# Optimization experiments

Measured on AMD Instinct MI355X. Metric: run time of the kernel, lower is better.

## Reference

```python
import jax, jax.numpy as jnp
import numpy as np
import math

# BDH config (defaults from BDHConfig)
D = 256        # n_embd
NH = 4         # n_head
MULT = 128     # mlp_internal_dim_multiplier
N = MULT * D // NH   # 8192 latent dim per head
NLAYER = 6
VOCAB = 256
B, T = 1, 1024
THETA = 2.0 ** 16
TWO_PI = 2.0 * math.pi


def _freqs(n):
    # get_freqs: quantize exponent to even integers
    t = jnp.arange(n, dtype=jnp.float32)
    q = jnp.floor(t / 2.0) * 2.0
    return 1.0 / (THETA ** (q / n)) / TWO_PI  # [N]


def _ln(x, eps=1e-5):
    # LayerNorm without affine params (elementwise_affine=False)
    m = jnp.mean(x, axis=-1, keepdims=True)
    v = jnp.mean((x - m) ** 2, axis=-1, keepdims=True)
    return (x - m) / jnp.sqrt(v + eps)


def _rope(phases, v):
    # phases: [T,N] broadcastable to v [...,T,N]
    ph = (phases % 1.0) * TWO_PI
    cos, sin = jnp.cos(ph), jnp.sin(ph)
    # rotate adjacent pairs: (-v_odd, v_even) interleaved
    vrot = jnp.stack((-v[..., 1::2], v[..., ::2]), axis=-1).reshape(v.shape)
    return v * cos + vrot * sin


def setup_inputs() -> dict:
    key = jax.random.key(0)
    ks = jax.random.split(key, 6)
    std = 0.02
    return {
        "idx": jax.random.randint(ks[0], (B, T), 0, VOCAB),
        "embed_w": jax.random.normal(ks[1], (VOCAB, D), jnp.float32) * std,
        "encoder": jax.random.normal(ks[2], (NH, D, N), jnp.float32) * std,
        "encoder_v": jax.random.normal(ks[3], (NH, D, N), jnp.float32) * std,
        "decoder": jax.random.normal(ks[4], (NH * N, D), jnp.float32) * std,
        "lm_head": jax.random.normal(ks[5], (D, VOCAB), jnp.float32) * std,
    }


def reference(idx, embed_w, encoder, encoder_v, decoder, lm_head):
    freqs = _freqs(N)                                             # [N]
    phases = jnp.arange(T, dtype=jnp.float32)[:, None] * freqs    # [T,N]
    mask = jnp.tril(jnp.ones((T, T), jnp.float32), k=-1)          # strict causal
    dec = decoder.reshape(NH, N, D)

    x = _ln(embed_w[idx])                                         # [B,T,D]
    for _ in range(NLAYER):
        x_sp = jax.nn.relu(jnp.einsum('btd,hdn->bhtn', x, encoder))   # [B,nh,T,N]
        qr = _rope(phases, x_sp)                                       # [B,nh,T,N]
        scores = jnp.einsum('bhtn,bhsn->bhts', qr, qr) * mask          # [B,nh,T,T]
        ykv = _ln(jnp.einsum('bhts,bsd->bhtd', scores, x))             # [B,nh,T,D]
        y_sp = jax.nn.relu(jnp.einsum('bhtd,hdn->bhtn', ykv, encoder_v))
        xy = x_sp * y_sp                                               # [B,nh,T,N]
        ymlp = jnp.einsum('bhtn,hnd->btd', xy, dec)                    # [B,T,D]
        x = _ln(x + _ln(ymlp))
    return x @ lm_head                                                 # [B,T,VOCAB]
```

## Files before the change

kernel.cpp:

```cpp
#include <hip/hip_runtime.h>
#include <hip/hip_bf16.h>
#include <math.h>

#define T_ 1024
#define D_ 256
#define N_ 8192
#define NH_ 4
#define NLAYER_ 6
#define VOCAB_ 256
#define TWO_PI_F 6.283185307179586f

typedef __attribute__((ext_vector_type(8))) short short8;
typedef __attribute__((ext_vector_type(4))) float floatx4;
typedef unsigned short ushort_t;

__device__ __forceinline__ void cp16(const void* g, void* l) {
    __builtin_amdgcn_global_load_lds((const __attribute__((address_space(1))) unsigned int*)g,
                                     (__attribute__((address_space(3))) unsigned int*)l,
                                     16, 0, 0);
}

__device__ __forceinline__ float bf2f_raw(unsigned short u) {
    union { unsigned int i; float f; } x;
    x.i = ((unsigned int)u) << 16;
    return x.f;
}
__device__ __forceinline__ unsigned int f2bf_u(float f) {
    union { float f; unsigned int u; } x; x.f = f;
    return (x.u + 0x7fffu + ((x.u >> 16) & 1u)) >> 16;
}
__device__ __forceinline__ unsigned int rope_fwd_w(unsigned int vw, unsigned int csw) {
    float ve = bf2f_raw((unsigned short)(vw & 0xffff));
    float vo = bf2f_raw((unsigned short)(vw >> 16));
    float c = bf2f_raw((unsigned short)(csw & 0xffff));
    float s = bf2f_raw((unsigned short)(csw >> 16));
    return f2bf_u(ve * c - vo * s) | (f2bf_u(vo * c + ve * s) << 16);
}
__device__ __forceinline__ unsigned int xy_mul_w(unsigned int vw, unsigned int qw,
                                                 unsigned int csw) {
    float ve = bf2f_raw((unsigned short)(vw & 0xffff));
    float vo = bf2f_raw((unsigned short)(vw >> 16));
    float qe = bf2f_raw((unsigned short)(qw & 0xffff));
    float qo = bf2f_raw((unsigned short)(qw >> 16));
    float c = bf2f_raw((unsigned short)(csw & 0xffff));
    float s = bf2f_raw((unsigned short)(csw >> 16));
    float xe = qe * c + qo * s;
    float xo = qo * c - qe * s;
    return f2bf_u(ve * xe) | (f2bf_u(vo * xo) << 16);
}

__device__ __forceinline__ float block_sum(float v, float* red) {
    int tid = threadIdx.x;
    red[tid] = v;
    __syncthreads();
    #pragma unroll
    for (int s = 128; s > 0; s >>= 1) {
        if (tid < s) red[tid] += red[tid + s];
        __syncthreads();
    }
    float r = red[0];
    __syncthreads();
    return r;
}


__global__ void k_embed_ln(const int* __restrict__ idx, const float* __restrict__ ew,
                           float* __restrict__ x, __hip_bfloat16* __restrict__ x_bf) {
    __shared__ float red[256];
    int t = blockIdx.x, d = threadIdx.x;
    float v = ew[idx[t] * D_ + d];
    float mean = block_sum(v, red) * (1.0f / D_);
    float c = v - mean;
    float var = block_sum(c * c, red) * (1.0f / D_);
    float o = c * rsqrtf(var + 1e-5f);
    x[t * D_ + d] = o;
    x_bf[t * D_ + d] = __float2bfloat16(o);
}

__global__ void k_ln_rows(const float* __restrict__ yp, __hip_bfloat16* __restrict__ outb) {
    __shared__ float red[256];
    int r = blockIdx.x, d = threadIdx.x;
    const size_t S = (size_t)NH_ * T_ * D_;
    float v = yp[(size_t)r * D_ + d] + yp[S + (size_t)r * D_ + d];
    float mean = block_sum(v, red) * (1.0f / D_);
    float c = v - mean;
    float var = block_sum(c * c, red) * (1.0f / D_);
    outb[(size_t)r * D_ + d] = __float2bfloat16(c * rsqrtf(var + 1e-5f));
}

__global__ void k_x_update(float* __restrict__ x, const unsigned int* __restrict__ ypart,
                           __hip_bfloat16* __restrict__ x_bf) {
    __shared__ float red[256];
    int t = blockIdx.x, d = threadIdx.x;
    float v = 0.0f;
    #pragma unroll
    for (int i = 0; i < 32; i++) {
        unsigned int w = ypart[(size_t)i * (T_ * D_ / 2) + t * (D_ / 2) + (d >> 1)];
        v += bf2f_raw((unsigned short)((d & 1) ? (w >> 16) : (w & 0xffff)));
    }
    float m1 = block_sum(v, red) * (1.0f / D_);
    float c1 = v - m1;
    float v1 = block_sum(c1 * c1, red) * (1.0f / D_);
    float u = c1 * rsqrtf(v1 + 1e-5f);
    float w = x[t * D_ + d] + u;
    float m2 = block_sum(w, red) * (1.0f / D_);
    float c2 = w - m2;
    float v2 = block_sum(c2 * c2, red) * (1.0f / D_);
    float o = c2 * rsqrtf(v2 + 1e-5f);
    x[t * D_ + d] = o;
    x_bf[t * D_ + d] = __float2bfloat16(o);
}

__global__ __launch_bounds__(256) void k_tcvt(const float* __restrict__ in,
                                              __hip_bfloat16* __restrict__ out,
                                              int R, int C) {
    int h = blockIdx.z;
    int r0 = blockIdx.y * 32, c0 = blockIdx.x * 32;
    __shared__ float tile[32][33];
    int tx = threadIdx.x & 31, ty = threadIdx.x >> 5;
    const float* inh = in + (size_t)h * R * C;
    __hip_bfloat16* outh = out + (size_t)h * R * C;
    #pragma unroll
    for (int i = 0; i < 4; i++)
        tile[ty + 8 * i][tx] = inh[(size_t)(r0 + ty + 8 * i) * C + c0 + tx];
    __syncthreads();
    #pragma unroll
    for (int i = 0; i < 4; i++)
        outh[(size_t)(c0 + ty + 8 * i) * R + r0 + tx] = __float2bfloat16(tile[tx][ty + 8 * i]);
}

__global__ void k_rope_tab(unsigned int* __restrict__ tab) {
    int idx = blockIdx.x * 256 + threadIdx.x;
    int t = idx >> 12, j = idx & 4095;
    float freq = exp2f((float)j * (-1.0f / 256.0f)) * 0.15915494309189535f;
    float ph = (float)t * freq;
    ph -= floorf(ph);
    float s, c;
    __sincosf(ph * TWO_PI_F, &s, &c);
    tab[idx] = f2bf_u(c) | (f2bf_u(s) << 16);
}

__device__ __forceinline__ void gemm128(const ushort_t* __restrict__ A,
                                        const ushort_t* __restrict__ B,
                                        int lda, int ldb, int K,
                                        ushort_t* As, ushort_t* Bs,
                                        floatx4 acc[4][4]) {
    const int tid = threadIdx.x;
    const int lane = tid & 63, wid = tid >> 6;
    const int wm = wid >> 1, wn = wid & 1;
    const int quad = lane >> 4, col = lane & 15;
    int srow[4], scol[4];
    #pragma unroll
    for (int i = 0; i < 4; i++) {
        int s = i * 256 + tid;
        srow[i] = s >> 3;
        scol[i] = (s & 7) ^ (srow[i] & 7);
    }
    for (int k0 = 0; k0 < K; k0 += 64) {
        #pragma unroll
        for (int i = 0; i < 4; i++)
            cp16(A + (size_t)srow[i] * lda + k0 + scol[i] * 8,
                 As + (size_t)(i * 256 + wid * 64) * 8);
        #pragma unroll
        for (int i = 0; i < 4; i++)
            cp16(B + (size_t)srow[i] * ldb + k0 + scol[i] * 8,
                 Bs + (size_t)(i * 256 + wid * 64) * 8);
        __syncthreads();
        #pragma unroll
        for (int kk = 0; kk < 2; kk++) {
            short8 af[4], bf[4];
            #pragma unroll
            for (int mi = 0; mi < 4; mi++) {
                int row = wm * 64 + mi * 16 + col;
                int pc = ((kk << 2) + quad) ^ (row & 7);
                af[mi] = *(const short8*)&As[row * 64 + pc * 8];
            }
            #pragma unroll
            for (int ni = 0; ni < 4; ni++) {
                int row = wn * 64 + ni * 16 + col;
                int pc = ((kk << 2) + quad) ^ (row & 7);
                bf[ni] = *(const short8*)&Bs[row * 64 + pc * 8];
            }
            #pragma unroll
            for (int mi = 0; mi < 4; mi++)
                #pragma unroll
                for (int ni = 0; ni < 4; ni++)
                    acc[mi][ni] = __builtin_amdgcn_mfma_f32_16x16x32_bf16(
                        af[mi], bf[ni], acc[mi][ni], 0, 0, 0);
        }
        __syncthreads();
    }
}

#define GEMM_PROLOGUE()                                              \
    __shared__ __align__(16) char smem[128 * 65 * 4];                \
    ushort_t* As = (ushort_t*)smem;                                  \
    ushort_t* Bs = (ushort_t*)(smem + 16384);                        \
    unsigned int* sst = (unsigned int*)smem;                         \
    floatx4 acc[4][4];                                               \
    _Pragma("unroll") for (int mi = 0; mi < 4; mi++)                 \
        _Pragma("unroll") for (int ni = 0; ni < 4; ni++)             \
            acc[mi][ni] = (floatx4){0.f, 0.f, 0.f, 0.f};             \
    const int lane = threadIdx.x & 63, wid = threadIdx.x >> 6;       \
    const int wm = wid >> 1, wn = wid & 1;                           \
    const int quad = lane >> 4, col = lane & 15;                     \
    const int odd = lane & 1;                                        \
    const int rsel = odd ? 2 : 0, rother = odd ? 0 : 2;

#define STAGE_PACKED(VALEXPR)                                                 \
    _Pragma("unroll") for (int mi = 0; mi < 4; mi++)                          \
        _Pragma("unroll") for (int ni = 0; ni < 4; ni++) {                    \
            const int w = wn * 32 + ni * 8 + (col >> 1);                      \
            const int lrb = wm * 64 + mi * 16 + quad * 4;                     \
            _Pragma("unroll") for (int rr = 0; rr < 2; rr++) {                \
                int lr_o = lrb + rother + rr;                                 \
                float send = (VALEXPR(acc[mi][ni][rother + rr], lr_o));       \
                float recv = __shfl_xor(send, 1);                             \
                int lr = lrb + rsel + rr;                                     \
                float mine = (VALEXPR(acc[mi][ni][rsel + rr], lr));           \
                float lo = odd ? recv : mine, hi = odd ? mine : recv;         \
                sst[lr * 65 + w] = f2bf_u(lo) | (f2bf_u(hi) << 16);           \
            }                                                                 \
        }                                                                     \
    __syncthreads();

__global__ __launch_bounds__(256) void k_scores_m(const __hip_bfloat16* __restrict__ qr,
                                                  __hip_bfloat16* __restrict__ scp) {
    const int b = blockIdx.x;
    const int ks = b & 3, h = (b >> 2) & 3;
    int i = b >> 4;
    int ti = 0;
    while ((ti + 1) * (ti + 2) / 2 <= i) ti++;
    int si = i - ti * (ti + 1) / 2;
    const int t0 = ti * 128, s0 = si * 128;
    GEMM_PROLOGUE();
    const ushort_t* qh = (const ushort_t*)qr + (size_t)h * T_ * N_ + (size_t)ks * (N_ / 4);
    gemm128(qh + (size_t)t0 * N_, qh + (size_t)s0 * N_, N_, N_, N_ / 4, As, Bs, acc);
    #pragma unroll
    for (int mi = 0; mi < 4; mi++)
        #pragma unroll
        for (int ni = 0; ni < 4; ni++) {
            const int ss = s0 + wn * 64 + ni * 16 + col;
            const int w = wn * 32 + ni * 8 + (col >> 1);
            const int lrb = wm * 64 + mi * 16 + quad * 4;
            #pragma unroll
            for (int rr = 0; rr < 2; rr++) {
                int lr_o = lrb + rother + rr;
                float send = (ss < t0 + lr_o) ? acc[mi][ni][rother + rr] : 0.0f;
                float recv = __shfl_xor(send, 1);
                int lr = lrb + rsel + rr;
                float mine = (ss < t0 + lr) ? acc[mi][ni][rsel + rr] : 0.0f;
                float lo = odd ? recv : mine, hi = odd ? mine : recv;
                sst[lr * 65 + w] = f2bf_u(lo) | (f2bf_u(hi) << 16);
            }
        }
    __syncthreads();
    unsigned int* gb = (unsigned int*)(scp + (size_t)ks * NH_ * T_ * T_ + (size_t)h * T_ * T_)
                       + (size_t)t0 * (T_ / 2) + (s0 >> 1);
    const int tid = threadIdx.x;
    #pragma unroll
    for (int p = 0; p < 8; p++) {
        int g = p * 1024 + tid * 4;
        int lr = g >> 6, w = g & 63;
        uint4 v = make_uint4(sst[lr * 65 + w], sst[lr * 65 + w + 1],
                             sst[lr * 65 + w + 2], sst[lr * 65 + w + 3]);
        *(uint4*)(gb + (size_t)lr * (T_ / 2) + w) = v;
    }
}

__global__ void k_sc_cvt(__hip_bfloat16* __restrict__ scp) {
    int i = blockIdx.x;
    int ti = 0;
    while ((ti + 1) * (ti + 2) / 2 <= i) ti++;
    int si = i - ti * (ti + 1) / 2;
    const size_t S2h = (size_t)NH_ * T_ * T_ / 2;
    unsigned int* sp = (unsigned int*)scp;
    size_t b = (size_t)blockIdx.y * T_ * T_ / 2;
    for (int e = threadIdx.x; e < 128 * 64; e += 256) {
        int r = e >> 6, c = e & 63;
        size_t off = b + (((size_t)(ti * 128 + r) * T_ + si * 128) >> 1) + c;
        float lo = 0.f, hi = 0.f;
        #pragma unroll
        for (int s = 0; s < 4; s++) {
            unsigned int w = sp[off + s * S2h];
            lo += bf2f_raw((unsigned short)(w & 0xffff));
            hi += bf2f_raw((unsigned short)(w >> 16));
        }
        sp[off] = f2bf_u(lo) | (f2bf_u(hi) << 16);
    }
}

#define IDENT_RELU(a, lr) fmaxf((a), 0.0f)
template <int MODE>
__global__ __launch_bounds__(256) void k_proj_m(const __hip_bfloat16* __restrict__ Abf,
                                                const __hip_bfloat16* __restrict__ Wt,
                                                __hip_bfloat16* __restrict__ out1,
                                                const unsigned int* __restrict__ rtab) {
    const int h = blockIdx.z;
    const int t0 = blockIdx.y * 128, n0 = blockIdx.x * 128;
    GEMM_PROLOGUE();
    const ushort_t* Ah = (const ushort_t*)Abf + (MODE ? (size_t)h * T_ * D_ : (size_t)0)
                         + (size_t)t0 * D_;
    const ushort_t* Bh = (const ushort_t*)Wt + (size_t)h * N_ * D_ + (size_t)n0 * D_;
    gemm128(Ah, Bh, D_, D_, D_, As, Bs, acc);
    STAGE_PACKED(IDENT_RELU);
    unsigned int* gb = (unsigned int*)out1 + ((size_t)h * T_ + t0) * (N_ / 2) + (n0 >> 1);
    const unsigned int* rb = rtab + (size_t)t0 * 4096 + (n0 >> 1);
    const int tid = threadIdx.x;
    #pragma unroll
    for (int p = 0; p < 8; p++) {
        int g = p * 1024 + tid * 4;
        int lr = g >> 6, w = g & 63;
        uint4 v = make_uint4(sst[lr * 65 + w], sst[lr * 65 + w + 1],
                             sst[lr * 65 + w + 2], sst[lr * 65 + w + 3]);
        uint4 cs = *(const uint4*)(rb + (size_t)lr * 4096 + w);
        uint4 o;
        if (MODE == 0) {
            o.x = rope_fwd_w(v.x, cs.x); o.y = rope_fwd_w(v.y, cs.y);
            o.z = rope_fwd_w(v.z, cs.z); o.w = rope_fwd_w(v.w, cs.w);
        } else {
            uint4 qw = *(const uint4*)(gb + (size_t)lr * (N_ / 2) + w);
            o.x = xy_mul_w(v.x, qw.x, cs.x); o.y = xy_mul_w(v.y, qw.y, cs.y);
            o.z = xy_mul_w(v.z, qw.z, cs.z); o.w = xy_mul_w(v.w, qw.w, cs.w);
        }
        *(uint4*)(gb + (size_t)lr * (N_ / 2) + w) = o;
    }
}

__global__ __launch_bounds__(256) void k_ykv_m(const __hip_bfloat16* __restrict__ sc,
                                               const __hip_bfloat16* __restrict__ xT,
                                               float* __restrict__ ykvp) {
    const int b = blockIdx.x;
    const int h = (b >> 1) & 3, ks = b & 1;
    const int r0 = b >> 3;
    const int d0 = (r0 & 1) * 128, t0 = (r0 >> 1) * 128;
    GEMM_PROLOGUE();
    const int half = (t0 + 128) >> 1;
    const ushort_t* Ah = (const ushort_t*)sc + (size_t)h * T_ * T_ + (size_t)t0 * T_ + ks * half;
    const ushort_t* Bh = (const ushort_t*)xT + (size_t)d0 * T_ + ks * half;
    gemm128(Ah, Bh, T_, T_, half, As, Bs, acc);
    float2* yp = (float2*)(ykvp + (size_t)ks * NH_ * T_ * D_);
    #pragma unroll
    for (int mi = 0; mi < 4; mi++)
        #pragma unroll
        for (int ni = 0; ni < 4; ni++) {
            const int dd_e = (d0 + wn * 64 + ni * 16 + col) & ~1;
            const int rowb = t0 + wm * 64 + mi * 16 + quad * 4;
            #pragma unroll
            for (int rr = 0; rr < 2; rr++) {
                float send = acc[mi][ni][rother + rr];
                float recv = __shfl_xor(send, 1);
                float mine = acc[mi][ni][rsel + rr];
                int tt = rowb + rsel + rr;
                yp[(((size_t)h * T_ + tt) * D_ + dd_e) >> 1] =
                    odd ? make_float2(recv, mine) : make_float2(mine, recv);
            }
        }
}

#define IDENT_PASS(a, lr) (a)
__global__ __launch_bounds__(256) void k_ymlp_m(const __hip_bfloat16* __restrict__ xy,
                                                const __hip_bfloat16* __restrict__ decT,
                                                unsigned int* __restrict__ ypart) {
    const int b = blockIdx.x;
    const int slice = b & 31;
    const int ks = slice >> 2, h = slice & 3;
    const int r0 = b >> 5;
    const int d0 = (r0 & 1) * 128, t0 = (r0 >> 1) * 128;
    GEMM_PROLOGUE();
    const ushort_t* Ah = (const ushort_t*)xy + (size_t)h * T_ * N_ + (size_t)t0 * N_ + ks * 1024;
    const ushort_t* Bh = (const ushort_t*)decT + (size_t)h * D_ * N_ + (size_t)d0 * N_ + ks * 1024;
    gemm128(Ah, Bh, N_, N_, 1024, As, Bs, acc);
    STAGE_PACKED(IDENT_PASS);
    unsigned int* gb = ypart + (size_t)slice * (T_ * D_ / 2) + (size_t)t0 * (D_ / 2) + (d0 >> 1);
    const int tid = threadIdx.x;
    #pragma unroll
    for (int p = 0; p < 8; p++) {
        int g = p * 1024 + tid * 4;
        int lr = g >> 6, w = g & 63;
        uint4 v = make_uint4(sst[lr * 65 + w], sst[lr * 65 + w + 1],
                             sst[lr * 65 + w + 2], sst[lr * 65 + w + 3]);
        *(uint4*)(gb + (size_t)lr * (D_ / 2) + w) = v;
    }
}

__global__ __launch_bounds__(256) void k_lmhead_m(const __hip_bfloat16* __restrict__ x_bf,
                                                  const __hip_bfloat16* __restrict__ lmT,
                                                  float* __restrict__ out) {
    const int v0 = blockIdx.x * 128, t0 = blockIdx.y * 128;
    GEMM_PROLOGUE();
    const ushort_t* Ah = (const ushort_t*)x_bf + (size_t)t0 * D_;
    const ushort_t* Bh = (const ushort_t*)lmT + (size_t)v0 * D_;
    gemm128(Ah, Bh, D_, D_, D_, As, Bs, acc);
    float2* op = (float2*)out;
    #pragma unroll
    for (int mi = 0; mi < 4; mi++)
        #pragma unroll
        for (int ni = 0; ni < 4; ni++) {
            const int vv_e = (v0 + wn * 64 + ni * 16 + col) & ~1;
            const int rowb = t0 + wm * 64 + mi * 16 + quad * 4;
            #pragma unroll
            for (int rr = 0; rr < 2; rr++) {
                float send = acc[mi][ni][rother + rr];
                float recv = __shfl_xor(send, 1);
                float mine = acc[mi][ni][rsel + rr];
                int tt = rowb + rsel + rr;
                op[((size_t)tt * VOCAB_ + vv_e) >> 1] =
                    odd ? make_float2(recv, mine) : make_float2(mine, recv);
            }
        }
}


extern "C" void kernel_launch(void* const* d_in, const int* in_sizes, int n_in,
                              void* d_out, int out_size, void* d_ws, size_t ws_size,
                              hipStream_t stream) {
    const int* idx = (const int*)d_in[0];
    const float* embed_w = (const float*)d_in[1];
    const float* encoder = (const float*)d_in[2];
    const float* encoder_v = (const float*)d_in[3];
    const float* decoder = (const float*)d_in[4];
    const float* lm_head = (const float*)d_in[5];
    float* out = (float*)d_out;

    char* p = (char*)d_ws;
    auto alloc = [&](size_t bytes) {
        char* q = p;
        p += (bytes + 255) & ~(size_t)255;
        return q;
    };
    float* x = (float*)alloc((size_t)T_ * D_ * 4);
    __hip_bfloat16* x_bf = (__hip_bfloat16*)alloc((size_t)T_ * D_ * 2);
    __hip_bfloat16* xT = (__hip_bfloat16*)alloc((size_t)T_ * D_ * 2);
    __hip_bfloat16* ykv_bf = (__hip_bfloat16*)alloc((size_t)NH_ * T_ * D_ * 2);
    __hip_bfloat16* scp = (__hip_bfloat16*)alloc((size_t)4 * NH_ * T_ * T_ * 2);
    __hip_bfloat16* qr = (__hip_bfloat16*)alloc((size_t)NH_ * T_ * N_ * 2);
    unsigned int* ypart = (unsigned int*)alloc((size_t)32 * T_ * D_ * 2);
    __hip_bfloat16* encT = (__hip_bfloat16*)alloc((size_t)NH_ * N_ * D_ * 2);
    __hip_bfloat16* encvT = (__hip_bfloat16*)alloc((size_t)NH_ * N_ * D_ * 2);
    __hip_bfloat16* decT = (__hip_bfloat16*)alloc((size_t)NH_ * N_ * D_ * 2);
    __hip_bfloat16* lmT = (__hip_bfloat16*)alloc((size_t)VOCAB_ * D_ * 2);
    unsigned int* rtab = (unsigned int*)alloc((size_t)T_ * 4096 * 4);
    float* ykvp = (float*)(scp + (size_t)NH_ * T_ * T_);

    k_tcvt<<<dim3(N_ / 32, D_ / 32, NH_), 256, 0, stream>>>(encoder, encT, D_, N_);
    k_tcvt<<<dim3(N_ / 32, D_ / 32, NH_), 256, 0, stream>>>(encoder_v, encvT, D_, N_);
    k_tcvt<<<dim3(D_ / 32, N_ / 32, NH_), 256, 0, stream>>>(decoder, decT, N_, D_);
    k_tcvt<<<dim3(VOCAB_ / 32, D_ / 32, 1), 256, 0, stream>>>(lm_head, lmT, D_, VOCAB_);
    k_rope_tab<<<T_ * 4096 / 256, 256, 0, stream>>>(rtab);

    k_embed_ln<<<T_, 256, 0, stream>>>(idx, embed_w, x, x_bf);
    for (int l = 0; l < NLAYER_; l++) {
        k_proj_m<0><<<dim3(N_ / 128, T_ / 128, NH_), 256, 0, stream>>>(x_bf, encT, qr, rtab);
        k_scores_m<<<36 * 16, 256, 0, stream>>>(qr, scp);
        k_sc_cvt<<<dim3(36, NH_), 256, 0, stream>>>(scp);
        k_tcvt<<<dim3(D_ / 32, T_ / 32, 1), 256, 0, stream>>>(x, xT, T_, D_);
        k_ykv_m<<<16 * 8, 256, 0, stream>>>(scp, xT, ykvp);
        k_ln_rows<<<NH_ * T_, 256, 0, stream>>>(ykvp, ykv_bf);
        k_proj_m<1><<<dim3(N_ / 128, T_ / 128, NH_), 256, 0, stream>>>(ykv_bf, encvT, qr, rtab);
        k_ymlp_m<<<16 * 32, 256, 0, stream>>>(qr, decT, ypart);
        k_x_update<<<T_, 256, 0, stream>>>(x, ypart, x_bf);
    }
    k_lmhead_m<<<dim3(VOCAB_ / 128, T_ / 128), 256, 0, stream>>>(x_bf, lmT, out);
}
```

Measured before the change: 1.327 ms.

## Fuse value projection, xy gating and decoder GEMM into one kernel

Replaces the separate value-projection kernel and decoder GEMM with one kernel. Each block computes a 128x128 chunk of relu(ykv@encoder_v), applies rope and the x_sp multiply in shared memory, then feeds that tile straight into the decoder MFMA accumulation. This avoids writing the large xy intermediate to global memory and reading it back. The price is that the value-projection GEMM is computed twice, once for each output column half, and the chunk loop is more serialised with extra barriers.

After: 1.744 ms. +31.4%, slower.

```diff
diff --git a/kernel.cpp b/kernel.cpp
--- a/kernel.cpp
+++ b/kernel.cpp
@@ -291,16 +291,14 @@
 }
 
 #define IDENT_RELU(a, lr) fmaxf((a), 0.0f)
-template <int MODE>
-__global__ __launch_bounds__(256) void k_proj_m(const __hip_bfloat16* __restrict__ Abf,
-                                                const __hip_bfloat16* __restrict__ Wt,
-                                                __hip_bfloat16* __restrict__ out1,
-                                                const unsigned int* __restrict__ rtab) {
+__global__ __launch_bounds__(256) void k_proj0_m(const __hip_bfloat16* __restrict__ Abf,
+                                                 const __hip_bfloat16* __restrict__ Wt,
+                                                 __hip_bfloat16* __restrict__ out1,
+                                                 const unsigned int* __restrict__ rtab) {
     const int h = blockIdx.z;
     const int t0 = blockIdx.y * 128, n0 = blockIdx.x * 128;
     GEMM_PROLOGUE();
-    const ushort_t* Ah = (const ushort_t*)Abf + (MODE ? (size_t)h * T_ * D_ : (size_t)0)
-                         + (size_t)t0 * D_;
+    const ushort_t* Ah = (const ushort_t*)Abf + (size_t)t0 * D_;
     const ushort_t* Bh = (const ushort_t*)Wt + (size_t)h * N_ * D_ + (size_t)n0 * D_;
     gemm128(Ah, Bh, D_, D_, D_, As, Bs, acc);
     STAGE_PACKED(IDENT_RELU);
@@ -315,14 +313,8 @@
                              sst[lr * 65 + w + 2], sst[lr * 65 + w + 3]);
         uint4 cs = *(const uint4*)(rb + (size_t)lr * 4096 + w);
         uint4 o;
-        if (MODE == 0) {
-            o.x = rope_fwd_w(v.x, cs.x); o.y = rope_fwd_w(v.y, cs.y);
-            o.z = rope_fwd_w(v.z, cs.z); o.w = rope_fwd_w(v.w, cs.w);
-        } else {
-            uint4 qw = *(const uint4*)(gb + (size_t)lr * (N_ / 2) + w);
-            o.x = xy_mul_w(v.x, qw.x, cs.x); o.y = xy_mul_w(v.y, qw.y, cs.y);
-            o.z = xy_mul_w(v.z, qw.z, cs.z); o.w = xy_mul_w(v.w, qw.w, cs.w);
-        }
+        o.x = rope_fwd_w(v.x, cs.x); o.y = rope_fwd_w(v.y, cs.y);
+        o.z = rope_fwd_w(v.z, cs.z); o.w = rope_fwd_w(v.w, cs.w);
         *(uint4*)(gb + (size_t)lr * (N_ / 2) + w) = o;
     }
 }
@@ -358,22 +350,138 @@
         }
 }
 
-#define IDENT_PASS(a, lr) (a)
-__global__ __launch_bounds__(256) void k_ymlp_m(const __hip_bfloat16* __restrict__ xy,
+__global__ __launch_bounds__(256, 2) void k_fvm(const __hip_bfloat16* __restrict__ ykv_bf,
+                                                const __hip_bfloat16* __restrict__ encvT,
                                                 const __hip_bfloat16* __restrict__ decT,
+                                                const __hip_bfloat16* __restrict__ qr,
+                                                const unsigned int* __restrict__ rtab,
                                                 unsigned int* __restrict__ ypart) {
     const int b = blockIdx.x;
-    const int slice = b & 31;
-    const int ks = slice >> 2, h = slice & 3;
-    const int r0 = b >> 5;
-    const int d0 = (r0 & 1) * 128, t0 = (r0 >> 1) * 128;
-    GEMM_PROLOGUE();
-    const ushort_t* Ah = (const ushort_t*)xy + (size_t)h * T_ * N_ + (size_t)t0 * N_ + ks * 1024;
-    const ushort_t* Bh = (const ushort_t*)decT + (size_t)h * D_ * N_ + (size_t)d0 * N_ + ks * 1024;
-    gemm128(Ah, Bh, N_, N_, 1024, As, Bs, acc);
-    STAGE_PACKED(IDENT_PASS);
-    unsigned int* gb = ypart + (size_t)slice * (T_ * D_ / 2) + (size_t)t0 * (D_ / 2) + (d0 >> 1);
+    const int slice = b & 63;
+    const int h = slice & 3;
+    const int npart = (slice >> 2) & 7;
+    const int d0 = (slice >> 5) & 1;
+    const int t0 = b >> 6;
+    __shared__ __align__(16) char smem[34816 + 16384];
+    ushort_t* As = (ushort_t*)smem;
+    ushort_t* Bs = (ushort_t*)(smem + 16384);
+    ushort_t* X = (ushort_t*)smem;
+    unsigned int* Xw = (unsigned int*)X;
+    ushort_t* B2s = (ushort_t*)(smem + 34816);
     const int tid = threadIdx.x;
+    const int lane = tid & 63, wid = tid >> 6;
+    const int wm = wid >> 1, wn = wid & 1;
+    const int quad = lane >> 4, col = lane & 15;
+    const int odd = lane & 1;
+    const int rsel = odd ? 2 : 0, rother = odd ? 0 : 2;
+    int srow[4], scol[4];
+    #pragma unroll
+    for (int i = 0; i < 4; i++) {
+        int s = i * 256 + tid;
+        srow[i] = s >> 3;
+        scol[i] = (s & 7) ^ (srow[i] & 7);
+    }
+    floatx4 acc2[4][4];
+    #pragma unroll
+    for (int mi = 0; mi < 4; mi++)
+        #pragma unroll
+        for (int ni = 0; ni < 4; ni++) acc2[mi][ni] = (floatx4){0.f, 0.f, 0.f, 0.f};
+
+    const ushort_t* Ah = (const ushort_t*)ykv_bf + ((size_t)h * T_ + t0 * 128) * D_;
+    const ushort_t* qrh = (const ushort_t*)qr + ((size_t)h * T_ + t0 * 128) * N_;
+
+    for (int c = 0; c < 8; c++) {
+        const int n0 = npart * 1024 + c * 128;
+        floatx4 acc1[4][4];
+        #pragma unroll
+        for (int mi = 0; mi < 4; mi++)
+            #pragma unroll
+            for (int ni = 0; ni < 4; ni++) acc1[mi][ni] = (floatx4){0.f, 0.f, 0.f, 0.f};
+        const ushort_t* Bh = (const ushort_t*)encvT + ((size_t)h * N_ + n0) * D_;
+        gemm128(Ah, Bh, D_, D_, D_, As, Bs, acc1);
+        #pragma unroll
+        for (int mi = 0; mi < 4; mi++)
+            #pragma unroll
+            for (int ni = 0; ni < 4; ni++) {
+                const int w = wn * 32 + ni * 8 + (col >> 1);
+                const int lrb = wm * 64 + mi * 16 + quad * 4;
+                #pragma unroll
+                for (int rr = 0; rr < 2; rr++) {
+                    float send = fmaxf(acc1[mi][ni][rother + rr], 0.0f);
+                    float recv = __shfl_xor(send, 1);
+                    int lr = lrb + rsel + rr;
+                    float mine = fmaxf(acc1[mi][ni][rsel + rr], 0.0f);
+                    float lo = odd ? recv : mine, hi = odd ? mine : recv;
+                    Xw[lr * 68 + w] = f2bf_u(lo) | (f2bf_u(hi) << 16);
+                }
+            }
+        __syncthreads();
+        #pragma unroll
+        for (int p = 0; p < 8; p++) {
+            int g = p * 1024 + tid * 4;
+            int lr = g >> 6, w = g & 63;
+            uint4 xv = *(uint4*)&Xw[lr * 68 + w];
+            uint4 qv = *(const uint4*)((const unsigned int*)(qrh + (size_t)lr * N_) +
+                                       (n0 >> 1) + w);
+            uint4 cv = *(const uint4*)(rtab + (size_t)(t0 * 128 + lr) * 4096 + (n0 >> 1) + w);
+            xv.x = xy_mul_w(xv.x, qv.x, cv.x);
+            xv.y = xy_mul_w(xv.y, qv.y, cv.y);
+            xv.z = xy_mul_w(xv.z, qv.z, cv.z);
+            xv.w = xy_mul_w(xv.w, qv.w, cv.w);
+            *(uint4*)&Xw[lr * 68 + w] = xv;
+        }
+        __syncthreads();
+        const ushort_t* B2 = (const ushort_t*)decT + ((size_t)h * D_ + d0 * 128) * N_ + n0;
+        for (int k2 = 0; k2 < 128; k2 += 64) {
+            #pragma unroll
+            for (int i = 0; i < 4; i++)
+                cp16(B2 + (size_t)srow[i] * N_ + k2 + scol[i] * 8,
+                     B2s + (size_t)(i * 256 + wid * 64) * 8);
+            __syncthreads();
+            #pragma unroll
+            for (int kk = 0; kk < 2; kk++) {
+                short8 af[4], bf[4];
+                #pragma unroll
+                for (int mi = 0; mi < 4; mi++) {
+                    int row = wm * 64 + mi * 16 + col;
+                    af[mi] = *(const short8*)&X[row * 136 + k2 + (kk * 4 + quad) * 8];
+                }
+                #pragma unroll
+                for (int ni = 0; ni < 4; ni++) {
+                    int row = wn * 64 + ni * 16 + col;
+                    int pc = ((kk << 2) + quad) ^ (row & 7);
+                    bf[ni] = *(const short8*)&B2s[row * 64 + pc * 8];
+                }
+                #pragma unroll
+                for (int mi = 0; mi < 4; mi++)
+                    #pragma unroll
+                    for (int ni = 0; ni < 4; ni++)
+                        acc2[mi][ni] = __builtin_amdgcn_mfma_f32_16x16x32_bf16(
+                            af[mi], bf[ni], acc2[mi][ni], 0, 0, 0);
+            }
+            __syncthreads();
+        }
+    }
+    unsigned int* sst = (unsigned int*)smem;
+    #pragma unroll
+    for (int mi = 0; mi < 4; mi++)
+        #pragma unroll
+        for (int ni = 0; ni < 4; ni++) {
+            const int w = wn * 32 + ni * 8 + (col >> 1);
+            const int lrb = wm * 64 + mi * 16 + quad * 4;
+            #pragma unroll
+            for (int rr = 0; rr < 2; rr++) {
+                float send = acc2[mi][ni][rother + rr];
+                float recv = __shfl_xor(send, 1);
+                int lr = lrb + rsel + rr;
+                float mine = acc2[mi][ni][rsel + rr];
+                float lo = odd ? recv : mine, hi = odd ? mine : recv;
+                sst[lr * 65 + w] = f2bf_u(lo) | (f2bf_u(hi) << 16);
+            }
+        }
+    __syncthreads();
+    unsigned int* gb = ypart + (size_t)(slice & 31) * (T_ * D_ / 2) +
+                       (size_t)(t0 * 128) * (D_ / 2) + d0 * 64;
     #pragma unroll
     for (int p = 0; p < 8; p++) {
         int g = p * 1024 + tid * 4;
@@ -451,14 +559,13 @@
 
     k_embed_ln<<<T_, 256, 0, stream>>>(idx, embed_w, x, x_bf);
     for (int l = 0; l < NLAYER_; l++) {
-        k_proj_m<0><<<dim3(N_ / 128, T_ / 128, NH_), 256, 0, stream>>>(x_bf, encT, qr, rtab);
+        k_proj0_m<<<dim3(N_ / 128, T_ / 128, NH_), 256, 0, stream>>>(x_bf, encT, qr, rtab);
         k_scores_m<<<36 * 16, 256, 0, stream>>>(qr, scp);
         k_sc_cvt<<<dim3(36, NH_), 256, 0, stream>>>(scp);
         k_tcvt<<<dim3(D_ / 32, T_ / 32, 1), 256, 0, stream>>>(x, xT, T_, D_);
         k_ykv_m<<<16 * 8, 256, 0, stream>>>(scp, xT, ykvp);
         k_ln_rows<<<NH_ * T_, 256, 0, stream>>>(ykvp, ykv_bf);
-        k_proj_m<1><<<dim3(N_ / 128, T_ / 128, NH_), 256, 0, stream>>>(ykv_bf, encvT, qr, rtab);
-        k_ymlp_m<<<16 * 32, 256, 0, stream>>>(qr, decT, ypart);
+        k_fvm<<<512, 256, 0, stream>>>(ykv_bf, encvT, decT, qr, rtab, ypart);
         k_x_update<<<T_, 256, 0, stream>>>(x, ypart, x_bf);
     }
     k_lmhead_m<<<dim3(VOCAB_ / 128, T_ / 128), 256, 0, stream>>>(x_bf, lmT, out);
```
